# Performance work log

Measured on AMD Instinct MI355X. Metric: run time of the kernel, lower is better.

## Reference

```python
import jax, jax.numpy as jnp
import numpy as np
import math

NEG = -1000000.0


def setup_inputs() -> dict:
    key = jax.random.key(0)
    ks = jax.random.split(key, 8)
    B, S, D = 4, 2048, 1024
    std = 1.0 / math.sqrt(D)
    return {
        "queries": jax.random.normal(ks[0], (B, S, D), jnp.float32),
        "keys": jax.random.normal(ks[1], (B, S, D), jnp.float32),
        "values": jax.random.normal(ks[2], (B, S, D), jnp.float32),
        "valid_len": jax.random.randint(ks[3], (B,), 1, S, dtype=jnp.int64 if jax.config.jax_enable_x64 else jnp.int32),
        "W_q": jax.random.normal(ks[4], (D, D), jnp.float32) * std,
        "W_k": jax.random.normal(ks[5], (D, D), jnp.float32) * std,
        "W_v": jax.random.normal(ks[6], (D, D), jnp.float32) * std,
        "W_o": jax.random.normal(ks[7], (D, D), jnp.float32) * std,
    }


def reference(queries, keys, values, valid_len, W_q, W_k, W_v, W_o):
    NUM_HEADS = 16
    B, S, D = queries.shape
    hd = D // NUM_HEADS

    def split_heads(x):
        # (B, S, D) -> (B, H, S, hd)
        return x.reshape(B, -1, NUM_HEADS, hd).transpose(0, 2, 1, 3)

    # nn.Linear with weight W applies x @ W.T
    q = split_heads(queries @ W_q.T)
    k = split_heads(keys @ W_k.T)
    v = split_heads(values @ W_v.T)

    scale = 1.0 / math.sqrt(hd)
    scores = jnp.einsum('bhqd,bhkd->bhqk', q, k) * scale  # (B, H, Sq, Sk)

    # key-padding mask from valid_len: positions >= valid_len are masked
    kpos = jnp.arange(scores.shape[-1])
    pad_mask = kpos[None, None, None, :] >= valid_len[:, None, None, None]
    scores = jnp.where(pad_mask, NEG, scores)
    attn = jax.nn.softmax(scores, axis=-1)

    out = jnp.einsum('bhqk,bhkd->bhqd', attn, v)  # (B, H, Sq, hd)
    out = out.transpose(0, 2, 1, 3).reshape(B, -1, D)
    return out @ W_o.T
```

## Files before the change

kernel.cpp:

```cpp
#include <hip/hip_runtime.h>
#include <hip/hip_bf16.h>

using bf16_t = __bf16;
using bf16x8 = __attribute__((ext_vector_type(8))) __bf16;
using bf16x4 = __attribute__((ext_vector_type(4))) __bf16;
using bf16x2 = __attribute__((ext_vector_type(2))) __bf16;
using f32x4  = __attribute__((ext_vector_type(4))) float;

#define S_  2048
#define D_  1024

typedef __attribute__((address_space(1))) unsigned int glb_u32;
typedef __attribute__((address_space(3))) unsigned int lds_u32;

__device__ __forceinline__ void async_cp16(const void* g, void* lds) {
    __builtin_amdgcn_global_load_lds(
        (glb_u32*)(unsigned long long)g,
        (lds_u32*)(unsigned int)(unsigned long long)lds,
        16, 0, 0);
}

__global__ __launch_bounds__(256) void cast_f32_bf16(const float* __restrict__ s,
                                                     bf16_t* __restrict__ d, int n4) {
    int i = blockIdx.x * 256 + threadIdx.x;
    if (i >= n4) return;
    float4 f = reinterpret_cast<const float4*>(s)[i];
    bf16x4 o;
    o[0] = (bf16_t)f.x; o[1] = (bf16_t)f.y; o[2] = (bf16_t)f.z; o[3] = (bf16_t)f.w;
    reinterpret_cast<bf16x4*>(d)[i] = o;
}

__global__ __launch_bounds__(256) void cast2_f32_bf16(const float* __restrict__ a, const float* __restrict__ b,
                                                      bf16_t* __restrict__ oa, bf16_t* __restrict__ ob, int n4) {
    int i = blockIdx.x * 256 + threadIdx.x;
    if (i >= n4) return;
    const float* s = blockIdx.y ? b : a;
    bf16_t*      d = blockIdx.y ? ob : oa;
    float4 f = reinterpret_cast<const float4*>(s)[i];
    bf16x4 o;
    o[0] = (bf16_t)f.x; o[1] = (bf16_t)f.y; o[2] = (bf16_t)f.z; o[3] = (bf16_t)f.w;
    reinterpret_cast<bf16x4*>(d)[i] = o;
}

__global__ __launch_bounds__(256) void cast4_f32_bf16(const float* __restrict__ a, const float* __restrict__ b,
                                                      const float* __restrict__ c, const float* __restrict__ dd,
                                                      bf16_t* __restrict__ oa, bf16_t* __restrict__ ob,
                                                      bf16_t* __restrict__ oc, bf16_t* __restrict__ od, int n4) {
    int i = blockIdx.x * 256 + threadIdx.x;
    if (i >= n4) return;
    const float* s; bf16_t* d;
    int w = blockIdx.y;
    if      (w == 0) { s = a;  d = oa; }
    else if (w == 1) { s = b;  d = ob; }
    else if (w == 2) { s = c;  d = oc; }
    else             { s = dd; d = od; }
    float4 f = reinterpret_cast<const float4*>(s)[i];
    bf16x4 o;
    o[0] = (bf16_t)f.x; o[1] = (bf16_t)f.y; o[2] = (bf16_t)f.z; o[3] = (bf16_t)f.w;
    reinterpret_cast<bf16x4*>(d)[i] = o;
}

template <int OUTMODE>
__global__ __launch_bounds__(256) void gemm_bt(const bf16_t* __restrict__ A,
                                               const bf16_t* __restrict__ Bt,
                                               void* __restrict__ Cv, float scale) {
    __shared__ bf16_t As[128 * 32];
    __shared__ bf16_t Bs[128 * 32];
    const int K = 1024;
    int tid  = threadIdx.x;
    int lane = tid & 63;
    int w    = tid >> 6;
    int l15  = lane & 15, quad = lane >> 4;
    int m0 = blockIdx.y * 128, n0 = blockIdx.x * 128;
    int wm = (w >> 1) * 64, wn = (w & 1) * 64;

    const bf16_t* Ag = A  + (size_t)(m0 + (tid >> 2)) * K + (tid & 3) * 8;
    const bf16_t* Bg = Bt + (size_t)(n0 + (tid >> 2)) * K + (tid & 3) * 8;
    bf16_t* Asw = As + tid * 8;
    bf16_t* Bsw = Bs + tid * 8;

    f32x4 acc[4][4] = {};

    for (int k0 = 0; k0 < K; k0 += 32) {
        __syncthreads();
        async_cp16(Ag + k0,                    Asw);
        async_cp16(Ag + k0 + (size_t)64 * K,   Asw + 2048);
        async_cp16(Bg + k0,                    Bsw);
        async_cp16(Bg + k0 + (size_t)64 * K,   Bsw + 2048);
        __syncthreads();
        bf16x8 af[4], bfr[4];
#pragma unroll
        for (int t = 0; t < 4; t++) {
            af[t]  = *reinterpret_cast<const bf16x8*>(&As[(wm + t * 16 + l15) * 32 + quad * 8]);
            bfr[t] = *reinterpret_cast<const bf16x8*>(&Bs[(wn + t * 16 + l15) * 32 + quad * 8]);
        }
#pragma unroll
        for (int mt = 0; mt < 4; mt++)
#pragma unroll
            for (int nt = 0; nt < 4; nt++)
                acc[mt][nt] = __builtin_amdgcn_mfma_f32_16x16x32_bf16(af[mt], bfr[nt], acc[mt][nt], 0, 0, 0);
    }

#pragma unroll
    for (int mt = 0; mt < 4; mt++)
#pragma unroll
        for (int nt = 0; nt < 4; nt++) {
            if (OUTMODE == 2) {
                int m = m0 + wm + mt * 16 + quad * 4;
                int n = n0 + wn + nt * 16 + l15;
                bf16x4 o4;
#pragma unroll
                for (int r = 0; r < 4; r++) o4[r] = (bf16_t)(acc[mt][nt][r] * scale);
                size_t vrow = (size_t)((m >> 11) * 16 + (n >> 6)) * 64 + (n & 63);
                *reinterpret_cast<bf16x4*>(&((bf16_t*)Cv)[vrow * S_ + (m & 2047)]) = o4;
            } else {
#pragma unroll
                for (int r = 0; r < 4; r++) {
                    int m = m0 + wm + mt * 16 + quad * 4 + r;
                    int n = n0 + wn + nt * 16 + l15;
                    size_t idx = (size_t)m * 1024 + n;
                    if (OUTMODE == 1) reinterpret_cast<float*>(Cv)[idx] = acc[mt][nt][r] * scale;
                    else              reinterpret_cast<bf16_t*>(Cv)[idx] = (bf16_t)(acc[mt][nt][r] * scale);
                }
            }
        }
}

__global__ __launch_bounds__(256) void attn_fused(const bf16_t* __restrict__ Qp,
                                                  const bf16_t* __restrict__ Kp,
                                                  const bf16_t* __restrict__ Vt,
                                                  const int* __restrict__ vlen_p,
                                                  bf16_t* __restrict__ Out) {
    __shared__ bf16_t Qs[2 * 128 * 32];
    __shared__ bf16_t Ks[2 * 64 * 32];
    __shared__ bf16_t Vs[64 * 68];

    int tid  = threadIdx.x;
    int lane = tid & 63, w = tid >> 6;
    int l15  = lane & 15, quad = lane >> 4;
    int qblk = blockIdx.x;
    int bh = blockIdx.y, b = bh >> 4, h = bh & 15;
    int vlen = vlen_p[b];
    int nkb  = (vlen + 63) >> 6;

    const bf16_t* Qg = Qp + (size_t)(b * S_ + qblk * 128) * D_ + h * 64;
    const bf16_t* Kg = Kp + (size_t)b * S_ * D_ + h * 64;
    const bf16_t* Vg = Vt + (size_t)bh * 64 * S_;

#pragma unroll
    for (int j = 0; j < 4; j++) {
        int linear = j * 256 + tid;
        int kk = linear >> 9, row = (linear >> 2) & 127, sub = linear & 3;
        async_cp16(Qg + (size_t)row * D_ + kk * 32 + sub * 8, Qs + linear * 8);
    }
    __syncthreads();
    bf16x8 qf[2][2];
#pragma unroll
    for (int qt = 0; qt < 2; qt++)
#pragma unroll
        for (int kk = 0; kk < 2; kk++)
            qf[qt][kk] = *reinterpret_cast<const bf16x8*>(&Qs[kk * 4096 + (w * 32 + qt * 16 + l15) * 32 + quad * 8]);

    f32x4 o[2][4] = {};
    float l_st[2] = {0.f, 0.f};

    for (int kb = 0; kb < nkb; kb++) {
        __syncthreads();
#pragma unroll
        for (int j = 0; j < 2; j++) {
            int linear = j * 256 + tid;
            int kk = linear >> 8, row = (linear >> 2) & 63, sub = linear & 3;
            async_cp16(Kg + (size_t)(kb * 64 + row) * D_ + kk * 32 + sub * 8, Ks + linear * 8);
        }
#pragma unroll
        for (int j = 0; j < 2; j++) {
            int linear = j * 256 + tid;
            int row = linear >> 3, c8 = linear & 7;
            uint4 vv = *reinterpret_cast<const uint4*>(&Vg[(size_t)row * S_ + kb * 64 + c8 * 8]);
            uint2* vp = reinterpret_cast<uint2*>(&Vs[row * 68 + c8 * 8]);
            vp[0] = make_uint2(vv.x, vv.y);
            vp[1] = make_uint2(vv.z, vv.w);
        }
        __syncthreads();

        f32x4 sc[2][4] = {};
#pragma unroll
        for (int nt = 0; nt < 4; nt++)
#pragma unroll
            for (int kk = 0; kk < 2; kk++) {
                bf16x8 kf = *reinterpret_cast<const bf16x8*>(&Ks[kk * 2048 + (nt * 16 + l15) * 32 + quad * 8]);
                sc[0][nt] = __builtin_amdgcn_mfma_f32_16x16x32_bf16(kf, qf[0][kk], sc[0][nt], 0, 0, 0);
                sc[1][nt] = __builtin_amdgcn_mfma_f32_16x16x32_bf16(kf, qf[1][kk], sc[1][nt], 0, 0, 0);
            }

        bool partial = (vlen & 63) && (kb == nkb - 1);
        bf16x8 pf[2][2];
        if (!partial) {
#pragma unroll
            for (int qt = 0; qt < 2; qt++) {
                float lacc = 0.f;
#pragma unroll
                for (int nt = 0; nt < 4; nt++)
#pragma unroll
                    for (int r = 0; r < 4; r++) {
                        float p = __builtin_exp2f(sc[qt][nt][r]);
                        lacc += p;
                        pf[qt][nt >> 1][(nt & 1) * 4 + r] = (bf16_t)p;
                    }
                l_st[qt] += lacc;
            }
        } else {
#pragma unroll
            for (int qt = 0; qt < 2; qt++) {
                float lacc = 0.f;
#pragma unroll
                for (int nt = 0; nt < 4; nt++)
#pragma unroll
                    for (int r = 0; r < 4; r++) {
                        float p = __builtin_exp2f(sc[qt][nt][r]);
                        if (kb * 64 + nt * 16 + quad * 4 + r >= vlen) p = 0.f;
                        lacc += p;
                        pf[qt][nt >> 1][(nt & 1) * 4 + r] = (bf16_t)p;
                    }
                l_st[qt] += lacc;
            }
        }

#pragma unroll
        for (int np = 0; np < 2; np++)
#pragma unroll
            for (int dt = 0; dt < 4; dt++) {
                bf16x4 v0 = *reinterpret_cast<const bf16x4*>(&Vs[(dt * 16 + l15) * 68 + np * 32 + quad * 4]);
                bf16x4 v1 = *reinterpret_cast<const bf16x4*>(&Vs[(dt * 16 + l15) * 68 + np * 32 + 16 + quad * 4]);
                bf16x8 vf;
#pragma unroll
                for (int j = 0; j < 4; j++) { vf[j] = v0[j]; vf[4 + j] = v1[j]; }
                o[0][dt] = __builtin_amdgcn_mfma_f32_16x16x32_bf16(vf, pf[0][np], o[0][dt], 0, 0, 0);
                o[1][dt] = __builtin_amdgcn_mfma_f32_16x16x32_bf16(vf, pf[1][np], o[1][dt], 0, 0, 0);
            }
    }

    float inv[2];
#pragma unroll
    for (int qt = 0; qt < 2; qt++) {
        float l = l_st[qt];
        l += __shfl_xor(l, 16);
        l += __shfl_xor(l, 32);
        inv[qt] = 1.0f / l;
    }

    __syncthreads();
    bf16_t* T = Qs;
#pragma unroll
    for (int qt = 0; qt < 2; qt++) {
        int row = w * 32 + qt * 16 + l15;
#pragma unroll
        for (int dt = 0; dt < 4; dt++) {
            int phys = ((dt * 2 + (quad >> 1)) ^ (l15 & 7));
            int base = row * 64 + phys * 8 + (quad & 1) * 4;
            bf16x2 t0, t1;
            t0[0] = (bf16_t)(o[qt][dt][0] * inv[qt]);
            t0[1] = (bf16_t)(o[qt][dt][1] * inv[qt]);
            t1[0] = (bf16_t)(o[qt][dt][2] * inv[qt]);
            t1[1] = (bf16_t)(o[qt][dt][3] * inv[qt]);
            *reinterpret_cast<bf16x2*>(&T[base])     = t0;
            *reinterpret_cast<bf16x2*>(&T[base + 2]) = t1;
        }
    }
    __syncthreads();
    {
        int row = w * 32 + (lane >> 1);
        int ch  = lane & 1;
        size_t orow = ((size_t)(b * S_ + qblk * 128) + row) * D_ + h * 64 + ch * 32;
#pragma unroll
        for (int k = 0; k < 4; k++) {
            int phys = (ch * 4 + k) ^ (row & 7);
            bf16x8 frag = *reinterpret_cast<const bf16x8*>(&T[row * 64 + phys * 8]);
            *reinterpret_cast<bf16x8*>(&Out[orow + k * 8]) = frag;
        }
    }
}

extern "C" void kernel_launch(void* const* d_in, const int* in_sizes, int n_in,
                              void* d_out, int out_size, void* d_ws, size_t ws_size,
                              hipStream_t stream) {
    const float* q  = (const float*)d_in[0];
    const float* k  = (const float*)d_in[1];
    const float* v  = (const float*)d_in[2];
    const int*   vl = (const int*)d_in[3];
    const float* Wq = (const float*)d_in[4];
    const float* Wk = (const float*)d_in[5];
    const float* Wv = (const float*)d_in[6];
    const float* Wo = (const float*)d_in[7];
    float* out = (float*)d_out;

    bf16_t* ws = (bf16_t*)d_ws;
    const size_t SD = (size_t)8192 * 1024;
    const size_t WW = (size_t)1024 * 1024;
    bf16_t* tmpA = ws;
    bf16_t* tmpB = ws + SD;
    bf16_t* Qp   = ws + 2 * SD;
    bf16_t* Kp   = ws + 3 * SD;
    bf16_t* Vt   = ws + 4 * SD;
    bf16_t* Wqb  = ws + 5 * SD;
    bf16_t* Wkb  = Wqb + WW;
    bf16_t* Wvb  = Wqb + 2 * WW;
    bf16_t* Wob  = Wqb + 3 * WW;

    const float cs = 0.18033688f;
    dim3 blk(256);
    dim3 gg(8, 64);

    cast4_f32_bf16<<<dim3(1024, 4), blk, 0, stream>>>(Wq, Wk, Wv, Wo, Wqb, Wkb, Wvb, Wob, 262144);
    cast2_f32_bf16<<<dim3(8192, 2), blk, 0, stream>>>(q, k, tmpA, tmpB, 2097152);

    gemm_bt<0><<<gg, blk, 0, stream>>>(tmpA, Wqb, Qp, cs);
    gemm_bt<0><<<gg, blk, 0, stream>>>(tmpB, Wkb, Kp, 1.0f);
    cast_f32_bf16<<<dim3(8192), blk, 0, stream>>>(v, tmpA, 2097152);
    gemm_bt<2><<<gg, blk, 0, stream>>>(tmpA, Wvb, Vt, 1.0f);

    attn_fused<<<dim3(16, 64), blk, 0, stream>>>(Qp, Kp, Vt, vl, tmpB);
    gemm_bt<1><<<gg, blk, 0, stream>>>(tmpB, Wob, out, 1.0f);
}
```

Baseline: 365.3 us.

## Fuse activation casts into batched QKV GEMM and trim attention LDS

Removes the separate fp32-to-bf16 cast kernels for q/k/v. The QKV projection GEMM now reads fp32 activations directly, converts them in registers and stores them to LDS, and it runs all three projections in one launch using blockIdx.z. The attention kernel loads Q fragments straight from global memory instead of staging them through LDS, shrinks its shared memory, and adds a min-blocks-per-CU hint of 5 for occupancy. The aim is to cut the extra global round-trips and launches, at the cost of synchronous fp32 A loads in the GEMM inner loop instead of async copies.

```diff
diff --git a/kernel.cpp b/kernel.cpp
--- a/kernel.cpp
+++ b/kernel.cpp
@@ -18,28 +18,6 @@
         (glb_u32*)(unsigned long long)g,
         (lds_u32*)(unsigned int)(unsigned long long)lds,
         16, 0, 0);
-}
-
-__global__ __launch_bounds__(256) void cast_f32_bf16(const float* __restrict__ s,
-                                                     bf16_t* __restrict__ d, int n4) {
-    int i = blockIdx.x * 256 + threadIdx.x;
-    if (i >= n4) return;
-    float4 f = reinterpret_cast<const float4*>(s)[i];
-    bf16x4 o;
-    o[0] = (bf16_t)f.x; o[1] = (bf16_t)f.y; o[2] = (bf16_t)f.z; o[3] = (bf16_t)f.w;
-    reinterpret_cast<bf16x4*>(d)[i] = o;
-}
-
-__global__ __launch_bounds__(256) void cast2_f32_bf16(const float* __restrict__ a, const float* __restrict__ b,
-                                                      bf16_t* __restrict__ oa, bf16_t* __restrict__ ob, int n4) {
-    int i = blockIdx.x * 256 + threadIdx.x;
-    if (i >= n4) return;
-    const float* s = blockIdx.y ? b : a;
-    bf16_t*      d = blockIdx.y ? ob : oa;
-    float4 f = reinterpret_cast<const float4*>(s)[i];
-    bf16x4 o;
-    o[0] = (bf16_t)f.x; o[1] = (bf16_t)f.y; o[2] = (bf16_t)f.z; o[3] = (bf16_t)f.w;
-    reinterpret_cast<bf16x4*>(d)[i] = o;
 }
 
 __global__ __launch_bounds__(256) void cast4_f32_bf16(const float* __restrict__ a, const float* __restrict__ b,
@@ -60,16 +38,97 @@
     reinterpret_cast<bf16x4*>(d)[i] = o;
 }
 
-template <int OUTMODE>
-__global__ __launch_bounds__(256) void gemm_bt(const bf16_t* __restrict__ A,
-                                               const bf16_t* __restrict__ Bt,
-                                               void* __restrict__ Cv, float scale) {
+__global__ __launch_bounds__(256) void gemm_qkv(const float* __restrict__ Aq, const float* __restrict__ Ak,
+                                                const float* __restrict__ Av,
+                                                const bf16_t* __restrict__ Wqb, const bf16_t* __restrict__ Wkb,
+                                                const bf16_t* __restrict__ Wvb,
+                                                bf16_t* __restrict__ Qp, bf16_t* __restrict__ Kp,
+                                                bf16_t* __restrict__ Vt, float cs) {
     __shared__ bf16_t As[128 * 32];
     __shared__ bf16_t Bs[128 * 32];
     const int K = 1024;
     int tid  = threadIdx.x;
-    int lane = tid & 63;
-    int w    = tid >> 6;
+    int lane = tid & 63, w = tid >> 6;
+    int l15  = lane & 15, quad = lane >> 4;
+    int z = blockIdx.z;
+    const float*  A  = (z == 0) ? Aq  : (z == 1) ? Ak  : Av;
+    const bf16_t* Bt = (z == 0) ? Wqb : (z == 1) ? Wkb : Wvb;
+    int m0 = blockIdx.y * 128, n0 = blockIdx.x * 128;
+    int wm = (w >> 1) * 64, wn = (w & 1) * 64;
+
+    int arow = tid >> 2, acol = (tid & 3) * 8;
+    const float*  Ag = A  + (size_t)(m0 + arow) * K + acol;
+    const bf16_t* Bg = Bt + (size_t)(n0 + (tid >> 2)) * K + (tid & 3) * 8;
+    bf16_t* Bsw = Bs + tid * 8;
+
+    f32x4 acc[4][4] = {};
+
+    for (int k0 = 0; k0 < K; k0 += 32) {
+        __syncthreads();
+        async_cp16(Bg + k0,                  Bsw);
+        async_cp16(Bg + k0 + (size_t)64 * K, Bsw + 2048);
+        float4 a0 = *reinterpret_cast<const float4*>(Ag + k0);
+        float4 a1 = *reinterpret_cast<const float4*>(Ag + k0 + 4);
+        float4 a2 = *reinterpret_cast<const float4*>(Ag + k0 + (size_t)64 * K);
+        float4 a3 = *reinterpret_cast<const float4*>(Ag + k0 + (size_t)64 * K + 4);
+        bf16x8 v0, v1;
+        v0[0]=(bf16_t)a0.x; v0[1]=(bf16_t)a0.y; v0[2]=(bf16_t)a0.z; v0[3]=(bf16_t)a0.w;
+        v0[4]=(bf16_t)a1.x; v0[5]=(bf16_t)a1.y; v0[6]=(bf16_t)a1.z; v0[7]=(bf16_t)a1.w;
+        v1[0]=(bf16_t)a2.x; v1[1]=(bf16_t)a2.y; v1[2]=(bf16_t)a2.z; v1[3]=(bf16_t)a2.w;
+        v1[4]=(bf16_t)a3.x; v1[5]=(bf16_t)a3.y; v1[6]=(bf16_t)a3.z; v1[7]=(bf16_t)a3.w;
+        *reinterpret_cast<bf16x8*>(&As[arow * 32 + acol])        = v0;
+        *reinterpret_cast<bf16x8*>(&As[(arow + 64) * 32 + acol]) = v1;
+        __syncthreads();
+        bf16x8 af[4], bfr[4];
+#pragma unroll
+        for (int t = 0; t < 4; t++) {
+            af[t]  = *reinterpret_cast<const bf16x8*>(&As[(wm + t * 16 + l15) * 32 + quad * 8]);
+            bfr[t] = *reinterpret_cast<const bf16x8*>(&Bs[(wn + t * 16 + l15) * 32 + quad * 8]);
+        }
+#pragma unroll
+        for (int mt = 0; mt < 4; mt++)
+#pragma unroll
+            for (int nt = 0; nt < 4; nt++)
+                acc[mt][nt] = __builtin_amdgcn_mfma_f32_16x16x32_bf16(af[mt], bfr[nt], acc[mt][nt], 0, 0, 0);
+    }
+
+    if (z == 2) {
+#pragma unroll
+        for (int mt = 0; mt < 4; mt++)
+#pragma unroll
+            for (int nt = 0; nt < 4; nt++) {
+                int m = m0 + wm + mt * 16 + quad * 4;
+                int n = n0 + wn + nt * 16 + l15;
+                bf16x4 o4;
+#pragma unroll
+                for (int r = 0; r < 4; r++) o4[r] = (bf16_t)acc[mt][nt][r];
+                size_t vrow = (size_t)((m >> 11) * 16 + (n >> 6)) * 64 + (n & 63);
+                *reinterpret_cast<bf16x4*>(&Vt[vrow * S_ + (m & 2047)]) = o4;
+            }
+    } else {
+        bf16_t* C = z ? Kp : Qp;
+        float scale = z ? 1.0f : cs;
+#pragma unroll
+        for (int mt = 0; mt < 4; mt++)
+#pragma unroll
+            for (int nt = 0; nt < 4; nt++)
+#pragma unroll
+                for (int r = 0; r < 4; r++) {
+                    int m = m0 + wm + mt * 16 + quad * 4 + r;
+                    int n = n0 + wn + nt * 16 + l15;
+                    C[(size_t)m * 1024 + n] = (bf16_t)(acc[mt][nt][r] * scale);
+                }
+    }
+}
+
+__global__ __launch_bounds__(256) void gemm_out(const bf16_t* __restrict__ A,
+                                                const bf16_t* __restrict__ Bt,
+                                                float* __restrict__ C) {
+    __shared__ bf16_t As[128 * 32];
+    __shared__ bf16_t Bs[128 * 32];
+    const int K = 1024;
+    int tid  = threadIdx.x;
+    int lane = tid & 63, w = tid >> 6;
     int l15  = lane & 15, quad = lane >> 4;
     int m0 = blockIdx.y * 128, n0 = blockIdx.x * 128;
     int wm = (w >> 1) * 64, wn = (w & 1) * 64;
@@ -104,36 +163,24 @@
 #pragma unroll
     for (int mt = 0; mt < 4; mt++)
 #pragma unroll
-        for (int nt = 0; nt < 4; nt++) {
-            if (OUTMODE == 2) {
-                int m = m0 + wm + mt * 16 + quad * 4;
+        for (int nt = 0; nt < 4; nt++)
+#pragma unroll
+            for (int r = 0; r < 4; r++) {
+                int m = m0 + wm + mt * 16 + quad * 4 + r;
                 int n = n0 + wn + nt * 16 + l15;
-                bf16x4 o4;
-#pragma unroll
-                for (int r = 0; r < 4; r++) o4[r] = (bf16_t)(acc[mt][nt][r] * scale);
-                size_t vrow = (size_t)((m >> 11) * 16 + (n >> 6)) * 64 + (n & 63);
-                *reinterpret_cast<bf16x4*>(&((bf16_t*)Cv)[vrow * S_ + (m & 2047)]) = o4;
-            } else {
-#pragma unroll
-                for (int r = 0; r < 4; r++) {
-                    int m = m0 + wm + mt * 16 + quad * 4 + r;
-                    int n = n0 + wn + nt * 16 + l15;
-                    size_t idx = (size_t)m * 1024 + n;
-                    if (OUTMODE == 1) reinterpret_cast<float*>(Cv)[idx] = acc[mt][nt][r] * scale;
-                    else              reinterpret_cast<bf16_t*>(Cv)[idx] = (bf16_t)(acc[mt][nt][r] * scale);
-                }
-            }
-        }
-}
-
-__global__ __launch_bounds__(256) void attn_fused(const bf16_t* __restrict__ Qp,
-                                                  const bf16_t* __restrict__ Kp,
-                                                  const bf16_t* __restrict__ Vt,
-                                                  const int* __restrict__ vlen_p,
-                                                  bf16_t* __restrict__ Out) {
-    __shared__ bf16_t Qs[2 * 128 * 32];
-    __shared__ bf16_t Ks[2 * 64 * 32];
-    __shared__ bf16_t Vs[64 * 68];
+                C[(size_t)m * 1024 + n] = acc[mt][nt][r];
+            }
+}
+
+__global__ __launch_bounds__(256, 5) void attn_fused(const bf16_t* __restrict__ Qp,
+                                                     const bf16_t* __restrict__ Kp,
+                                                     const bf16_t* __restrict__ Vt,
+                                                     const int* __restrict__ vlen_p,
+                                                     bf16_t* __restrict__ Out) {
+    __shared__ bf16_t lds[8448];
+    bf16_t* Ks = lds;
+    bf16_t* Vs = lds + 4096;
+    bf16_t* T  = lds;
 
     int tid  = threadIdx.x;
     int lane = tid & 63, w = tid >> 6;
@@ -147,19 +194,13 @@
     const bf16_t* Kg = Kp + (size_t)b * S_ * D_ + h * 64;
     const bf16_t* Vg = Vt + (size_t)bh * 64 * S_;
 
-#pragma unroll
-    for (int j = 0; j < 4; j++) {
-        int linear = j * 256 + tid;
-        int kk = linear >> 9, row = (linear >> 2) & 127, sub = linear & 3;
-        async_cp16(Qg + (size_t)row * D_ + kk * 32 + sub * 8, Qs + linear * 8);
-    }
-    __syncthreads();
     bf16x8 qf[2][2];
 #pragma unroll
     for (int qt = 0; qt < 2; qt++)
 #pragma unroll
         for (int kk = 0; kk < 2; kk++)
-            qf[qt][kk] = *reinterpret_cast<const bf16x8*>(&Qs[kk * 4096 + (w * 32 + qt * 16 + l15) * 32 + quad * 8]);
+            qf[qt][kk] = *reinterpret_cast<const bf16x8*>(
+                &Qg[(size_t)(w * 32 + qt * 16 + l15) * D_ + kk * 32 + quad * 8]);
 
     f32x4 o[2][4] = {};
     float l_st[2] = {0.f, 0.f};
@@ -250,7 +291,6 @@
     }
 
     __syncthreads();
-    bf16_t* T = Qs;
 #pragma unroll
     for (int qt = 0; qt < 2; qt++) {
         int row = w * 32 + qt * 16 + l15;
@@ -297,28 +337,20 @@
     bf16_t* ws = (bf16_t*)d_ws;
     const size_t SD = (size_t)8192 * 1024;
     const size_t WW = (size_t)1024 * 1024;
-    bf16_t* tmpA = ws;
-    bf16_t* tmpB = ws + SD;
-    bf16_t* Qp   = ws + 2 * SD;
-    bf16_t* Kp   = ws + 3 * SD;
-    bf16_t* Vt   = ws + 4 * SD;
-    bf16_t* Wqb  = ws + 5 * SD;
+    bf16_t* Qp   = ws;
+    bf16_t* Kp   = ws + SD;
+    bf16_t* Vt   = ws + 2 * SD;
+    bf16_t* tmpO = ws + 3 * SD;
+    bf16_t* Wqb  = ws + 4 * SD;
     bf16_t* Wkb  = Wqb + WW;
     bf16_t* Wvb  = Wqb + 2 * WW;
     bf16_t* Wob  = Wqb + 3 * WW;
 
     const float cs = 0.18033688f;
     dim3 blk(256);
-    dim3 gg(8, 64);
 
     cast4_f32_bf16<<<dim3(1024, 4), blk, 0, stream>>>(Wq, Wk, Wv, Wo, Wqb, Wkb, Wvb, Wob, 262144);
-    cast2_f32_bf16<<<dim3(8192, 2), blk, 0, stream>>>(q, k, tmpA, tmpB, 2097152);
-
-    gemm_bt<0><<<gg, blk, 0, stream>>>(tmpA, Wqb, Qp, cs);
-    gemm_bt<0><<<gg, blk, 0, stream>>>(tmpB, Wkb, Kp, 1.0f);
-    cast_f32_bf16<<<dim3(8192), blk, 0, stream>>>(v, tmpA, 2097152);
-    gemm_bt<2><<<gg, blk, 0, stream>>>(tmpA, Wvb, Vt, 1.0f);
-
-    attn_fused<<<dim3(16, 64), blk, 0, stream>>>(Qp, Kp, Vt, vl, tmpB);
-    gemm_bt<1><<<gg, blk, 0, stream>>>(tmpB, Wob, out, 1.0f);
-}
+    gemm_qkv<<<dim3(8, 64, 3), blk, 0, stream>>>(q, k, v, Wqb, Wkb, Wvb, Qp, Kp, Vt, cs);
+    attn_fused<<<dim3(16, 64), blk, 0, stream>>>(Qp, Kp, Vt, vl, tmpO);
+    gemm_out<<<dim3(8, 64), blk, 0, stream>>>(tmpO, Wob, out);
+}
```

New measurement: 469.1 us. +28.4%, slower.
